# Kernel tuning notes

Measured on AMD Instinct MI355X. Metric: run time of the kernel, lower is better.

Reference implementation:

```python
import jax, jax.numpy as jnp
import numpy as np


def setup_inputs() -> dict:
    key = jax.random.key(0)
    ks = jax.random.split(key, 7)
    B, N, K, D = 256, 50, 12, 128
    return {
        "batch_size": B,
        "itm_emb": jax.random.normal(ks[0], (B, N, D), jnp.float32),
        "ave_sess_itms_emb": jax.random.normal(ks[1], (B, N, D), jnp.float32),
        "glob_adj_itm_embs": jax.random.normal(ks[2], (B, N, K, D), jnp.float32),
        "glob_adj_wgt_embs": jax.random.normal(ks[3], (B, N, K), jnp.float32),
        "w1": jax.random.normal(ks[4], (D + 1, D), jnp.float32) * 0.1,
        "w2": jax.random.normal(ks[5], (D, 1), jnp.float32) * 0.1,
        "w3": jax.random.normal(ks[6], (2 * D, D), jnp.float32) * 0.1,
    }


def reference(batch_size, itm_emb, ave_sess_itms_emb, glob_adj_itm_embs,
              glob_adj_wgt_embs, w1, w2, w3):
    D = itm_emb.shape[-1]
    # [B,N,1,D] * [B,N,K,D] -> [B,N,K,D]; concat weight -> [B,N,K,D+1]
    alpha = ave_sess_itms_emb[:, :, None, :] * glob_adj_itm_embs
    alpha = jnp.concatenate([alpha, glob_adj_wgt_embs[..., None]], axis=-1)
    alpha = jnp.einsum('bnkc,cd->bnkd', alpha, w1)          # [B,N,K,D]
    alpha = jax.nn.leaky_relu(alpha, negative_slope=0.2)
    alpha = jnp.einsum('bnkd,do->bnk', alpha, w2)           # [B,N,K]
    alpha = jax.nn.softmax(alpha, axis=-1)[..., None]       # [B,N,K,1]
    att = jnp.sum(alpha * glob_adj_itm_embs, axis=-2)       # [B,N,D]
    g = jnp.concatenate([itm_emb, att], axis=-1)            # [B,N,2D]
    # dropout with p=0.0 / eval mode is identity
    g = jnp.einsum('bnc,cd->bnd', g, w3)
    g = g.reshape(batch_size, -1, D)
    return jax.nn.relu(g)
```

## Files before the change

### kernel.cpp

```cpp
#include <hip/hip_runtime.h>

#define DD 128
#define KADJ 12
#define BN_TOTAL 12800

typedef float f32x4 __attribute__((ext_vector_type(4)));
typedef float f32x2 __attribute__((ext_vector_type(2)));
typedef __bf16 bf16x8 __attribute__((ext_vector_type(8)));
typedef __bf16 bf16x2 __attribute__((ext_vector_type(2)));
typedef unsigned int u32;

__device__ __forceinline__ bf16x8 cvt8(f32x4 a, f32x4 b) {
    bf16x8 r;
    r[0] = (__bf16)a[0]; r[1] = (__bf16)a[1]; r[2] = (__bf16)a[2]; r[3] = (__bf16)a[3];
    r[4] = (__bf16)b[0]; r[5] = (__bf16)b[1]; r[6] = (__bf16)b[2]; r[7] = (__bf16)b[3];
    return r;
}

__device__ __forceinline__ bf16x8 mul8(bf16x8 a, bf16x8 b) {
    bf16x8 r;
    #pragma unroll
    for (int i = 0; i < 8; ++i) r[i] = (__bf16)((float)a[i] * (float)b[i]);
    return r;
}

__global__ void k_prep(const float* __restrict__ w1, const float* __restrict__ w3,
                       __bf16* __restrict__ w1f, __bf16* __restrict__ w3f) {
    int idx = blockIdx.x * 256 + threadIdx.x;
    int lane = (idx >> 3) & 63, e = idx & 7;
    int l = lane & 15, gg = lane >> 4;
    if (idx < 16384) {
        int fi = idx >> 9, n = fi >> 2, ks = fi & 3;
        int k = ks * 32 + gg * 8 + e;
        w1f[idx] = (__bf16)w1[k * DD + n * 16 + l];
    } else {
        int j = idx - 16384;
        int fi = j >> 9, n = fi >> 3, ks = fi & 7;
        int k = ks * 32 + gg * 8 + e;
        w3f[j] = (__bf16)w3[k * DD + n * 16 + l];
    }
}

__launch_bounds__(256, 4)
__global__ void k_att(const float* __restrict__ ave, const float* __restrict__ adj,
                      const float* __restrict__ wgt, const float* __restrict__ w1,
                      const float* __restrict__ w2, const __bf16* __restrict__ w1f,
                      float* __restrict__ att_out) {
    __shared__ unsigned char lds[48 * 256 + 4 * 272 + 48 * 4];
    unsigned char* adjb = lds;
    unsigned char* aveb = lds + 48 * 256;
    float* sco = (float*)(lds + 48 * 256 + 4 * 272);

    const int t = threadIdx.x;
    const int lane = t & 63;
    const int w = t >> 6;
    const int l = lane & 15, g = lane >> 4;
    const int Bn0 = blockIdx.x * 4;
    const size_t R0 = (size_t)Bn0 * KADJ;

    #pragma unroll
    for (int i = 0; i < 3; ++i) {
        int idx = i * 256 + t;
        int row = idx >> 4, c8 = idx & 15;
        const float* gs = adj + (R0 + row) * (size_t)DD + c8 * 8;
        f32x4 v0 = *reinterpret_cast<const f32x4*>(gs);
        f32x4 v1 = *reinterpret_cast<const f32x4*>(gs + 4);
        *reinterpret_cast<bf16x8*>(adjb + row * 256 + ((c8 ^ (row & 15)) << 4)) =
            cvt8(v0, v1);
    }
    {
        f32x2 v = *reinterpret_cast<const f32x2*>(ave + (size_t)(Bn0 + w) * DD + lane * 2);
        bf16x2 bv; bv[0] = (__bf16)v[0]; bv[1] = (__bf16)v[1];
        *reinterpret_cast<bf16x2*>(aveb + w * 272 + lane * 4) = bv;
    }
    __syncthreads();

    {
        const int lr = w * 12 + (l < KADJ ? l : KADJ - 1);
        f32x4 acc[8];
        #pragma unroll
        for (int n = 0; n < 8; ++n) acc[n] = f32x4{0.f, 0.f, 0.f, 0.f};
        #pragma unroll 1
        for (int ks = 0; ks < 4; ++ks) {
            bf16x8 bq[8];
            #pragma unroll
            for (int n = 0; n < 8; ++n)
                bq[n] = *reinterpret_cast<const bf16x8*>(
                    w1f + ((size_t)(n * 4 + ks) * 512 + lane * 8));
            bf16x8 adjf = *reinterpret_cast<const bf16x8*>(
                adjb + lr * 256 + (((ks * 4 + g) ^ (lr & 15)) << 4));
            bf16x8 avef = *reinterpret_cast<const bf16x8*>(
                aveb + w * 272 + ks * 64 + g * 16);
            bf16x8 af = mul8(adjf, avef);
            #pragma unroll
            for (int n = 0; n < 8; ++n)
                acc[n] = __builtin_amdgcn_mfma_f32_16x16x32_bf16(af, bq[n], acc[n], 0, 0, 0);
        }
        float wv[4];
        #pragma unroll
        for (int j = 0; j < 4; ++j)
            wv[j] = (g < 3) ? wgt[R0 + (size_t)w * 12 + g * 4 + j] : 0.f;
        float p[4] = {0.f, 0.f, 0.f, 0.f};
        #pragma unroll
        for (int n = 0; n < 8; ++n) {
            float w1rn = w1[128 * DD + n * 16 + l];
            float w2vn = w2[n * 16 + l];
            #pragma unroll
            for (int j = 0; j < 4; ++j) {
                float h = fmaf(wv[j], w1rn, acc[n][j]);
                h = h > 0.f ? h : 0.2f * h;
                p[j] = fmaf(h, w2vn, p[j]);
            }
        }
        #pragma unroll
        for (int j = 0; j < 4; ++j) {
            p[j] += __shfl_xor(p[j], 1, 64);
            p[j] += __shfl_xor(p[j], 2, 64);
            p[j] += __shfl_xor(p[j], 4, 64);
            p[j] += __shfl_xor(p[j], 8, 64);
        }
        if (l == 0 && g < 3)
            *reinterpret_cast<f32x4*>(&sco[w * 12 + g * 4]) =
                f32x4{p[0], p[1], p[2], p[3]};
    }
    __syncthreads();

    {
        float s[KADJ];
        float mx = -1e30f;
        #pragma unroll
        for (int k = 0; k < KADJ; ++k) { s[k] = sco[w * 12 + k]; mx = fmaxf(mx, s[k]); }
        float ssum = 0.f;
        #pragma unroll
        for (int k = 0; k < KADJ; ++k) { s[k] = __expf(s[k] - mx); ssum += s[k]; }
        float inv = 1.f / ssum;
        float a0 = 0.f, a1 = 0.f;
        #pragma unroll
        for (int k = 0; k < KADJ; ++k) {
            int row = w * 12 + k;
            u32 pk = *reinterpret_cast<const u32*>(
                adjb + row * 256 + (((lane >> 2) ^ (row & 15)) << 4) + (lane & 3) * 4);
            float alpha = s[k] * inv;
            float e0 = __builtin_bit_cast(float, pk << 16);
            float e1 = __builtin_bit_cast(float, pk & 0xFFFF0000u);
            a0 = fmaf(alpha, e0, a0);
            a1 = fmaf(alpha, e1, a1);
        }
        *reinterpret_cast<f32x2*>(att_out + (size_t)(Bn0 + w) * DD + lane * 2) =
            f32x2{a0, a1};
    }
}

__launch_bounds__(256)
__global__ void k_out(const float* __restrict__ itm, const float* att,
                      const __bf16* __restrict__ w3f, float* outp) {
    const int t = threadIdx.x;
    const int lane = t & 63;
    const int w = t >> 6;
    const int l = lane & 15, g = lane >> 4;
    const int R0 = blockIdx.x * 64 + w * 16;
    const int row = R0 + l;

    bf16x8 afr[8];
    const float* ip = itm + (size_t)row * DD;
    #pragma unroll
    for (int s = 0; s < 4; ++s) {
        int c = s * 32 + g * 8;
        f32x4 a0 = *reinterpret_cast<const f32x4*>(ip + c);
        f32x4 a1 = *reinterpret_cast<const f32x4*>(ip + c + 4);
        afr[s] = cvt8(a0, a1);
    }
    const float* ap = att + (size_t)row * DD;
    #pragma unroll
    for (int s = 0; s < 4; ++s) {
        int c = s * 32 + g * 8;
        f32x4 a0 = *reinterpret_cast<const f32x4*>(ap + c);
        f32x4 a1 = *reinterpret_cast<const f32x4*>(ap + c + 4);
        afr[4 + s] = cvt8(a0, a1);
    }

    f32x4 acc[8];
    #pragma unroll
    for (int n = 0; n < 8; ++n) acc[n] = f32x4{0.f, 0.f, 0.f, 0.f};
    #pragma unroll
    for (int s = 0; s < 8; ++s) {
        const __bf16* bp = w3f + ((size_t)s * 64 + lane) * 8;
        #pragma unroll
        for (int n = 0; n < 8; ++n) {
            bf16x8 bfr = *reinterpret_cast<const bf16x8*>(bp + (size_t)n * 4096);
            acc[n] = __builtin_amdgcn_mfma_f32_16x16x32_bf16(afr[s], bfr, acc[n], 0, 0, 0);
        }
    }

    #pragma unroll
    for (int n = 0; n < 8; ++n) {
        #pragma unroll
        for (int j = 0; j < 4; ++j)
            outp[(size_t)(R0 + g * 4 + j) * DD + n * 16 + l] = fmaxf(acc[n][j], 0.f);
    }
}

extern "C" void kernel_launch(void* const* d_in, const int* in_sizes, int n_in,
                              void* d_out, int out_size, void* d_ws, size_t ws_size,
                              hipStream_t stream) {
    const float* itm = (const float*)d_in[1];
    const float* ave = (const float*)d_in[2];
    const float* adj = (const float*)d_in[3];
    const float* wgt = (const float*)d_in[4];
    const float* w1  = (const float*)d_in[5];
    const float* w2  = (const float*)d_in[6];
    const float* w3  = (const float*)d_in[7];
    float* outp = (float*)d_out;

    __bf16* w1f = (__bf16*)d_ws;
    __bf16* w3f = (__bf16*)((char*)d_ws + 32 * 1024);

    k_prep<<<dim3(192), dim3(256), 0, stream>>>(w1, w3, w1f, w3f);
    k_att<<<dim3(BN_TOTAL / 4), dim3(256), 0, stream>>>(ave, adj, wgt, w1, w2, w1f, outp);
    k_out<<<dim3(BN_TOTAL / 64), dim3(256), 0, stream>>>(itm, outp, w3f, outp);
}
```

Baseline: 47.82 us.

## Pipeline adjacency loads with double-buffered LDS and stage W1 fragments in LDS

The attention kernel now handles 16 (b,n) items per block in four groups of four. The global loads for the next group are issued into registers while the current group is computed, and LDS is double-buffered. W1 bf16 fragments are copied once per block into LDS instead of being read from global memory in every k-step, and only 3 waves run the MFMA since 48 rows fit in three 16-row tiles. This aims to hide HBM latency and cut redundant weight traffic, but it uses about 58KB of LDS, which limits occupancy to a couple of blocks per CU, and gives 4x fewer blocks.

```diff
diff --git a/kernel.cpp b/kernel.cpp
--- a/kernel.cpp
+++ b/kernel.cpp
@@ -7,7 +7,6 @@
 typedef float f32x4 __attribute__((ext_vector_type(4)));
 typedef float f32x2 __attribute__((ext_vector_type(2)));
 typedef __bf16 bf16x8 __attribute__((ext_vector_type(8)));
-typedef __bf16 bf16x2 __attribute__((ext_vector_type(2)));
 typedef unsigned int u32;
 
 __device__ __forceinline__ bf16x8 cvt8(f32x4 a, f32x4 b) {
@@ -41,114 +40,141 @@
     }
 }
 
-__launch_bounds__(256, 4)
+__launch_bounds__(256, 2)
 __global__ void k_att(const float* __restrict__ ave, const float* __restrict__ adj,
                       const float* __restrict__ wgt, const float* __restrict__ w1,
                       const float* __restrict__ w2, const __bf16* __restrict__ w1f,
                       float* __restrict__ att_out) {
-    __shared__ unsigned char lds[48 * 256 + 4 * 272 + 48 * 4];
-    unsigned char* adjb = lds;
-    unsigned char* aveb = lds + 48 * 256;
-    float* sco = (float*)(lds + 48 * 256 + 4 * 272);
+    __shared__ unsigned char lds[59584];
+    __bf16* w1s = (__bf16*)lds;
+    float* sco = (float*)(lds + 59392);
 
     const int t = threadIdx.x;
     const int lane = t & 63;
     const int w = t >> 6;
-    const int l = lane & 15, g = lane >> 4;
-    const int Bn0 = blockIdx.x * 4;
-    const size_t R0 = (size_t)Bn0 * KADJ;
-
-    #pragma unroll
-    for (int i = 0; i < 3; ++i) {
-        int idx = i * 256 + t;
-        int row = idx >> 4, c8 = idx & 15;
-        const float* gs = adj + (R0 + row) * (size_t)DD + c8 * 8;
-        f32x4 v0 = *reinterpret_cast<const f32x4*>(gs);
-        f32x4 v1 = *reinterpret_cast<const f32x4*>(gs + 4);
-        *reinterpret_cast<bf16x8*>(adjb + row * 256 + ((c8 ^ (row & 15)) << 4)) =
-            cvt8(v0, v1);
-    }
+    const int l = lane & 15, gq = lane >> 4;
+    const int bn_base = blockIdx.x * 16;
+
     {
-        f32x2 v = *reinterpret_cast<const f32x2*>(ave + (size_t)(Bn0 + w) * DD + lane * 2);
-        bf16x2 bv; bv[0] = (__bf16)v[0]; bv[1] = (__bf16)v[1];
-        *reinterpret_cast<bf16x2*>(aveb + w * 272 + lane * 4) = bv;
-    }
-    __syncthreads();
-
-    {
-        const int lr = w * 12 + (l < KADJ ? l : KADJ - 1);
-        f32x4 acc[8];
-        #pragma unroll
-        for (int n = 0; n < 8; ++n) acc[n] = f32x4{0.f, 0.f, 0.f, 0.f};
-        #pragma unroll 1
-        for (int ks = 0; ks < 4; ++ks) {
-            bf16x8 bq[8];
-            #pragma unroll
-            for (int n = 0; n < 8; ++n)
-                bq[n] = *reinterpret_cast<const bf16x8*>(
-                    w1f + ((size_t)(n * 4 + ks) * 512 + lane * 8));
-            bf16x8 adjf = *reinterpret_cast<const bf16x8*>(
-                adjb + lr * 256 + (((ks * 4 + g) ^ (lr & 15)) << 4));
-            bf16x8 avef = *reinterpret_cast<const bf16x8*>(
-                aveb + w * 272 + ks * 64 + g * 16);
-            bf16x8 af = mul8(adjf, avef);
-            #pragma unroll
-            for (int n = 0; n < 8; ++n)
-                acc[n] = __builtin_amdgcn_mfma_f32_16x16x32_bf16(af, bq[n], acc[n], 0, 0, 0);
-        }
-        float wv[4];
-        #pragma unroll
-        for (int j = 0; j < 4; ++j)
-            wv[j] = (g < 3) ? wgt[R0 + (size_t)w * 12 + g * 4 + j] : 0.f;
-        float p[4] = {0.f, 0.f, 0.f, 0.f};
-        #pragma unroll
-        for (int n = 0; n < 8; ++n) {
-            float w1rn = w1[128 * DD + n * 16 + l];
-            float w2vn = w2[n * 16 + l];
+        const f32x4* src = (const f32x4*)w1f;
+        f32x4* dst = (f32x4*)w1s;
+        #pragma unroll
+        for (int p = 0; p < 8; ++p) dst[p * 256 + t] = src[p * 256 + t];
+    }
+
+    f32x4 pa[6], pe0, pe1;
+    const int s_row = t >> 4, s_c8 = t & 15;
+    #define ISSUE(G) do {                                                         \
+        size_t rb_ = ((size_t)bn_base + (G) * 4) * KADJ;                          \
+        _Pragma("unroll")                                                         \
+        for (int i_ = 0; i_ < 3; ++i_) {                                          \
+            const float* gs_ = adj + (rb_ + i_ * 16 + s_row) * DD + s_c8 * 8;     \
+            pa[2 * i_]     = *reinterpret_cast<const f32x4*>(gs_);                \
+            pa[2 * i_ + 1] = *reinterpret_cast<const f32x4*>(gs_ + 4);            \
+        }                                                                         \
+        if (t < 64) {                                                             \
+            const float* as_ = ave + ((size_t)bn_base + (G) * 4 + (t >> 4)) * DD  \
+                               + (t & 15) * 8;                                    \
+            pe0 = *reinterpret_cast<const f32x4*>(as_);                           \
+            pe1 = *reinterpret_cast<const f32x4*>(as_ + 4);                       \
+        }                                                                         \
+    } while (0)
+
+    ISSUE(0);
+
+    #pragma unroll 1
+    for (int gi = 0; gi < 4; ++gi) {
+        unsigned char* bufA = lds + 32768 + (gi & 1) * 12288;
+        unsigned char* bufV = lds + 57344 + (gi & 1) * 1024;
+
+        #pragma unroll
+        for (int i = 0; i < 3; ++i) {
+            int row = i * 16 + s_row;
+            *reinterpret_cast<bf16x8*>(
+                bufA + row * 256 + ((s_c8 ^ (row & 15)) << 4)) =
+                cvt8(pa[2 * i], pa[2 * i + 1]);
+        }
+        if (t < 64)
+            *reinterpret_cast<bf16x8*>(bufV + (t >> 4) * 256 + (t & 15) * 16) =
+                cvt8(pe0, pe1);
+        if (gi < 3) ISSUE(gi + 1);
+        __syncthreads();
+
+        if (w < 3) {
+            const int lr = w * 16 + l;
+            const int bnl = lr / 12;
+            f32x4 acc[8];
+            #pragma unroll
+            for (int n = 0; n < 8; ++n) acc[n] = f32x4{0.f, 0.f, 0.f, 0.f};
+            #pragma unroll 1
+            for (int ks = 0; ks < 4; ++ks) {
+                bf16x8 adjf = *reinterpret_cast<const bf16x8*>(
+                    bufA + lr * 256 + (((ks * 4 + gq) ^ (lr & 15)) << 4));
+                bf16x8 avef = *reinterpret_cast<const bf16x8*>(
+                    bufV + bnl * 256 + ks * 64 + gq * 16);
+                bf16x8 af = mul8(adjf, avef);
+                #pragma unroll
+                for (int n = 0; n < 8; ++n) {
+                    bf16x8 bq = *reinterpret_cast<const bf16x8*>(
+                        w1s + (size_t)(n * 4 + ks) * 512 + lane * 8);
+                    acc[n] = __builtin_amdgcn_mfma_f32_16x16x32_bf16(af, bq, acc[n], 0, 0, 0);
+                }
+            }
+            float wv[4];
+            #pragma unroll
+            for (int j = 0; j < 4; ++j)
+                wv[j] = wgt[((size_t)bn_base + gi * 4) * KADJ + w * 16 + gq * 4 + j];
+            float p[4] = {0.f, 0.f, 0.f, 0.f};
+            #pragma unroll
+            for (int n = 0; n < 8; ++n) {
+                float w1rn = w1[128 * DD + n * 16 + l];
+                float w2vn = w2[n * 16 + l];
+                #pragma unroll
+                for (int j = 0; j < 4; ++j) {
+                    float h = fmaf(wv[j], w1rn, acc[n][j]);
+                    h = h > 0.f ? h : 0.2f * h;
+                    p[j] = fmaf(h, w2vn, p[j]);
+                }
+            }
             #pragma unroll
             for (int j = 0; j < 4; ++j) {
-                float h = fmaf(wv[j], w1rn, acc[n][j]);
-                h = h > 0.f ? h : 0.2f * h;
-                p[j] = fmaf(h, w2vn, p[j]);
-            }
-        }
-        #pragma unroll
-        for (int j = 0; j < 4; ++j) {
-            p[j] += __shfl_xor(p[j], 1, 64);
-            p[j] += __shfl_xor(p[j], 2, 64);
-            p[j] += __shfl_xor(p[j], 4, 64);
-            p[j] += __shfl_xor(p[j], 8, 64);
-        }
-        if (l == 0 && g < 3)
-            *reinterpret_cast<f32x4*>(&sco[w * 12 + g * 4]) =
-                f32x4{p[0], p[1], p[2], p[3]};
-    }
-    __syncthreads();
-
-    {
-        float s[KADJ];
-        float mx = -1e30f;
-        #pragma unroll
-        for (int k = 0; k < KADJ; ++k) { s[k] = sco[w * 12 + k]; mx = fmaxf(mx, s[k]); }
-        float ssum = 0.f;
-        #pragma unroll
-        for (int k = 0; k < KADJ; ++k) { s[k] = __expf(s[k] - mx); ssum += s[k]; }
-        float inv = 1.f / ssum;
-        float a0 = 0.f, a1 = 0.f;
-        #pragma unroll
-        for (int k = 0; k < KADJ; ++k) {
-            int row = w * 12 + k;
-            u32 pk = *reinterpret_cast<const u32*>(
-                adjb + row * 256 + (((lane >> 2) ^ (row & 15)) << 4) + (lane & 3) * 4);
-            float alpha = s[k] * inv;
-            float e0 = __builtin_bit_cast(float, pk << 16);
-            float e1 = __builtin_bit_cast(float, pk & 0xFFFF0000u);
-            a0 = fmaf(alpha, e0, a0);
-            a1 = fmaf(alpha, e1, a1);
-        }
-        *reinterpret_cast<f32x2*>(att_out + (size_t)(Bn0 + w) * DD + lane * 2) =
-            f32x2{a0, a1};
-    }
+                p[j] += __shfl_xor(p[j], 1, 64);
+                p[j] += __shfl_xor(p[j], 2, 64);
+                p[j] += __shfl_xor(p[j], 4, 64);
+                p[j] += __shfl_xor(p[j], 8, 64);
+            }
+            if (l == 0)
+                *reinterpret_cast<f32x4*>(&sco[w * 16 + gq * 4]) =
+                    f32x4{p[0], p[1], p[2], p[3]};
+        }
+        __syncthreads();
+
+        {
+            float s[KADJ];
+            float mx = -1e30f;
+            #pragma unroll
+            for (int k = 0; k < KADJ; ++k) { s[k] = sco[w * 12 + k]; mx = fmaxf(mx, s[k]); }
+            float ssum = 0.f;
+            #pragma unroll
+            for (int k = 0; k < KADJ; ++k) { s[k] = __expf(s[k] - mx); ssum += s[k]; }
+            float inv = 1.f / ssum;
+            float a0 = 0.f, a1 = 0.f;
+            #pragma unroll
+            for (int k = 0; k < KADJ; ++k) {
+                int row = w * 12 + k;
+                u32 pk = *reinterpret_cast<const u32*>(
+                    bufA + row * 256 + (((lane >> 2) ^ (row & 15)) << 4) + (lane & 3) * 4);
+                float alpha = s[k] * inv;
+                float e0 = __builtin_bit_cast(float, pk << 16);
+                float e1 = __builtin_bit_cast(float, pk & 0xFFFF0000u);
+                a0 = fmaf(alpha, e0, a0);
+                a1 = fmaf(alpha, e1, a1);
+            }
+            *reinterpret_cast<f32x2*>(
+                att_out + ((size_t)bn_base + gi * 4 + w) * DD + lane * 2) = f32x2{a0, a1};
+        }
+    }
+    #undef ISSUE
 }
 
 __launch_bounds__(256)
@@ -216,6 +242,6 @@
     __bf16* w3f = (__bf16*)((char*)d_ws + 32 * 1024);
 
     k_prep<<<dim3(192), dim3(256), 0, stream>>>(w1, w3, w1f, w3f);
-    k_att<<<dim3(BN_TOTAL / 4), dim3(256), 0, stream>>>(ave, adj, wgt, w1, w2, w1f, outp);
+    k_att<<<dim3(BN_TOTAL / 16), dim3(256), 0, stream>>>(ave, adj, wgt, w1, w2, w1f, outp);
     k_out<<<dim3(BN_TOTAL / 64), dim3(256), 0, stream>>>(itm, outp, w3f, outp);
 }
```

Measured after the change: 48.57 us. Within noise of the previous version (+1.6%).
